# Kernel tuning notes

Measured on AMD Instinct MI355X. Metric: run time of the kernel, lower is better.

Reference implementation:

```python
import jax, jax.numpy as jnp
import numpy as np

N = 50000   # num_nodes
F = 128     # node_features
E = 800000  # num_edges (avg degree 16)


def setup_inputs() -> dict:
    key = jax.random.key(0)
    ks = jax.random.split(key, 12)
    s = 1.0 / np.sqrt(F)
    return {
        "x": jax.random.normal(ks[0], (N, F), jnp.float32),
        "edge_index": jax.random.randint(ks[1], (2, E), 0, N),
        "edge_weight": jax.random.uniform(ks[2], (E,), jnp.float32),
        # TopKPooling projection vector p (PyG stores it as [1, F])
        "p": jax.random.normal(ks[3], (F,), jnp.float32) * s,
        # GRU params, torch gate order (r, z, n)
        "w_ih": jax.random.normal(ks[4], (3 * F, F), jnp.float32) * s,
        "w_hh": jax.random.normal(ks[5], (3 * F, F), jnp.float32) * s,
        "b_ih": jax.random.normal(ks[6], (3 * F,), jnp.float32) * s,
        "b_hh": jax.random.normal(ks[7], (3 * F,), jnp.float32) * s,
        # initial evolving GCN weight [F, F] (glorot-initialized in original)
        "W0": jax.random.normal(ks[8], (F, F), jnp.float32) * s,
        # trailing Linear(F, F)
        "W_lin": jax.random.normal(ks[9], (F, F), jnp.float32) * s,
        "b_lin": jax.random.normal(ks[10], (F,), jnp.float32) * s,
    }


def reference(x, edge_index, edge_weight, p, w_ih, w_hh, b_ih, b_hh, W0, W_lin, b_lin):
    n_nodes, f = x.shape
    # --- TopKPooling: score nodes, select top-F (ratio = F/N) ---
    score = jnp.tanh((x @ p) / jnp.linalg.norm(p))          # [N]
    top_scores, perm = jax.lax.top_k(score, f)              # sorted desc, k = F
    x_tilde = x[perm] * top_scores[:, None]                 # [F, F]
    # --- GRU single step (seq_len=1, batch=F): evolve weight matrix ---
    gi = x_tilde @ w_ih.T + b_ih                            # [F, 3F]
    gh = W0 @ w_hh.T + b_hh                                 # [F, 3F]
    r = jax.nn.sigmoid(gi[:, :f] + gh[:, :f])
    z = jax.nn.sigmoid(gi[:, f:2 * f] + gh[:, f:2 * f])
    n = jnp.tanh(gi[:, 2 * f:] + r * gh[:, 2 * f:])
    W = (1.0 - z) * n + z * W0                              # evolved [F, F]
    # --- GCNConv_Fixed_W: gcn_norm (self-loops, sym norm) + aggregate ---
    loop = jnp.arange(n_nodes)
    row = jnp.concatenate([edge_index[0], loop])            # sources
    col = jnp.concatenate([edge_index[1], loop])            # targets
    ew = jnp.concatenate([edge_weight, jnp.ones((n_nodes,), x.dtype)])
    deg = jax.ops.segment_sum(ew, col, num_segments=n_nodes)
    dinv = jnp.where(deg > 0, jnp.where(deg > 0, deg, 1.0) ** -0.5, 0.0)
    norm = dinv[row] * ew * dinv[col]                       # [E+N]
    xw = x @ W                                              # [N, F]
    h = jax.ops.segment_sum(norm[:, None] * xw[row], col, num_segments=n_nodes)
    # --- relu + Linear ---
    return jax.nn.relu(h) @ W_lin.T + b_lin
```

## Files before the change

kernel.cpp:

```cpp
#include <hip/hip_runtime.h>
#include <hip/hip_fp16.h>

#define NF 128
#define TK 128

typedef _Float16 f16;
typedef f16 half8 __attribute__((ext_vector_type(8)));
typedef float floatx4 __attribute__((ext_vector_type(4)));

__device__ __forceinline__ unsigned okey(float f) {
  unsigned u = __float_as_uint(f);
  return (u & 0x80000000u) ? ~u : (u | 0x80000000u);
}

__device__ __forceinline__ void edge_slice(const int* __restrict__ ei, const float* __restrict__ ew,
                                           unsigned long long* __restrict__ cnt64,
                                           unsigned short* __restrict__ eslot, int E, int e, int elim) {
  if (e < elim) {
    int c = ei[E + e];
    unsigned fx = __float2uint_rn(ew[e] * 16777216.0f);
    unsigned long long old =
        atomicAdd(&cnt64[c], ((unsigned long long)1 << 32) | (unsigned long long)fx);
    eslot[e] = (unsigned short)(old >> 32);
  }
}

__global__ void score_kernel(const float* __restrict__ x, const float* __restrict__ p,
                             float* __restrict__ score, unsigned* __restrict__ keys,
                             unsigned* __restrict__ bins, int n) {
  int t = threadIdx.x;
  int rib = t >> 3;
  int l8 = t & 7;
  int r = blockIdx.x * 32 + rib;
  if (r >= n) return;
  const float4* xr = (const float4*)&x[(size_t)r * NF + l8 * 16];
  const float4* pr = (const float4*)&p[l8 * 16];
  float d = 0.f, pp = 0.f;
#pragma unroll
  for (int i = 0; i < 4; ++i) {
    float4 xv = xr[i];
    float4 pv = pr[i];
    d = fmaf(xv.x, pv.x, d); d = fmaf(xv.y, pv.y, d);
    d = fmaf(xv.z, pv.z, d); d = fmaf(xv.w, pv.w, d);
    pp = fmaf(pv.x, pv.x, pp); pp = fmaf(pv.y, pv.y, pp);
    pp = fmaf(pv.z, pv.z, pp); pp = fmaf(pv.w, pv.w, pp);
  }
#pragma unroll
  for (int off = 4; off > 0; off >>= 1) {
    d += __shfl_down(d, off, 8);
    pp += __shfl_down(pp, off, 8);
  }
  if (l8 == 0) {
    float s = tanhf(d / sqrtf(pp));
    score[r] = s;
    unsigned k = okey(s);
    keys[r] = k;
    atomicAdd(&bins[k >> 16], 1u);
  }
}

__global__ __launch_bounds__(1024) void findbin_edge_kernel(const unsigned* __restrict__ bins,
                                                            unsigned* __restrict__ thrB,
                                                            const int* __restrict__ ei,
                                                            const float* __restrict__ ew,
                                                            unsigned long long* __restrict__ cnt64,
                                                            unsigned short* __restrict__ eslot,
                                                            int E, int ebase, int elim) {
  if (blockIdx.x > 0) {
    edge_slice(ei, ew, cnt64, eslot, E, ebase + ((int)blockIdx.x - 1) * 1024 + (int)threadIdx.x, elim);
    return;
  }
  __shared__ unsigned csum[1024];
  int t = threadIdx.x;
  unsigned hv[64];
  unsigned s = 0;
  const unsigned* bp = bins + t * 64;
#pragma unroll
  for (int b = 0; b < 64; ++b) { hv[b] = bp[b]; s += hv[b]; }
  csum[t] = s;
  __syncthreads();
  for (int st = 1; st < 1024; st <<= 1) {
    unsigned add = (t + st < 1024) ? csum[t + st] : 0u;
    __syncthreads();
    csum[t] += add;
    __syncthreads();
  }
  unsigned mySum = csum[t];
  unsigned above = (t == 1023) ? 0u : csum[t + 1];
  if (mySum >= (unsigned)TK && above < (unsigned)TK) {
    unsigned cum = above;
    int b = 63;
    for (; b > 0; --b) {
      unsigned h = hv[b];
      if (cum + h >= (unsigned)TK) break;
      cum += h;
    }
    thrB[0] = (unsigned)(t * 64 + b);
  }
}

__global__ __launch_bounds__(1024) void compact_edge_kernel(const unsigned* __restrict__ keys,
                                                            const unsigned* __restrict__ thrB,
                                                            int* __restrict__ ncnt,
                                                            int* __restrict__ candIdx, int n, int nOwn,
                                                            const int* __restrict__ ei,
                                                            const float* __restrict__ ew,
                                                            unsigned long long* __restrict__ cnt64,
                                                            unsigned short* __restrict__ eslot,
                                                            int E, int ebase, int elim) {
  if ((int)blockIdx.x >= nOwn) {
    edge_slice(ei, ew, cnt64, eslot, E,
               ebase + ((int)blockIdx.x - nOwn) * 1024 + (int)threadIdx.x, elim);
    return;
  }
  int i = blockIdx.x * 1024 + threadIdx.x;
  if (i < n) {
    if ((keys[i] >> 16) >= thrB[0]) {
      int pos = atomicAdd(ncnt, 1);
      candIdx[pos] = i;
    }
  }
}

#define CCAP 6144
__global__ __launch_bounds__(1024) void select_edge_kernel(const unsigned* __restrict__ keys,
                                                           const int* __restrict__ candIdx,
                                                           const int* __restrict__ ncp,
                                                           const float* __restrict__ score,
                                                           int* __restrict__ perm,
                                                           float* __restrict__ tsc,
                                                           const int* __restrict__ ei,
                                                           const float* __restrict__ ew,
                                                           unsigned long long* __restrict__ cnt64,
                                                           unsigned short* __restrict__ eslot,
                                                           int E, int ebase, int elim) {
  if (blockIdx.x > 0) {
    edge_slice(ei, ew, cnt64, eslot, E, ebase + ((int)blockIdx.x - 1) * 1024 + (int)threadIdx.x, elim);
    return;
  }
  __shared__ unsigned sk[CCAP];
  __shared__ int si[CCAP];
  int nc = ncp[0];
  int t = threadIdx.x;
  int m = nc < CCAP ? nc : CCAP;
  for (int i = t; i < m; i += 1024) {
    int ci = candIdx[i];
    si[i] = ci;
    sk[i] = keys[ci];
  }
  __syncthreads();
  for (int ci = t; ci < nc; ci += 1024) {
    unsigned mk;
    int mi;
    if (ci < CCAP) { mk = sk[ci]; mi = si[ci]; }
    else { mi = candIdx[ci]; mk = keys[mi]; }
    int rank = 0;
    for (int j = 0; j < m; ++j) {
      unsigned kj = sk[j];
      int ij = si[j];
      rank += (kj > mk || (kj == mk && ij < mi)) ? 1 : 0;
    }
    for (int j = CCAP; j < nc; ++j) {
      int ij = candIdx[j];
      unsigned kj = keys[ij];
      rank += (kj > mk || (kj == mk && ij < mi)) ? 1 : 0;
    }
    if (rank < TK) {
      perm[rank] = mi;
      tsc[rank] = score[mi];
    }
  }
}

__global__ void gru_edge_kernel(const float* __restrict__ x, const int* __restrict__ perm,
                                const float* __restrict__ tsc, const float* __restrict__ W0,
                                const float* __restrict__ w_ih, const float* __restrict__ w_hh,
                                const float* __restrict__ b_ih, const float* __restrict__ b_hh,
                                float* __restrict__ WT,
                                const int* __restrict__ ei, const float* __restrict__ ew,
                                unsigned long long* __restrict__ cnt64,
                                unsigned short* __restrict__ eslot, int E, int ebase, int elim) {
  if ((int)blockIdx.x >= NF) {
    edge_slice(ei, ew, cnt64, eslot, E, ebase + ((int)blockIdx.x - NF) * 128 + (int)threadIdx.x, elim);
    return;
  }
  __shared__ float xs[NF], w0s[NF];
  int i = blockIdx.x, j = threadIdx.x;
  int pi = perm[i];
  float s = tsc[i];
  xs[j] = x[(size_t)pi * NF + j] * s;
  w0s[j] = W0[i * NF + j];
  __syncthreads();
  float gir = b_ih[j], giz = b_ih[NF + j], gin = b_ih[2 * NF + j];
  float ghr = b_hh[j], ghz = b_hh[NF + j], ghn = b_hh[2 * NF + j];
  const float* wr = w_ih + (size_t)j * NF;
  const float* wz = w_ih + (size_t)(NF + j) * NF;
  const float* wn = w_ih + (size_t)(2 * NF + j) * NF;
  const float* ur = w_hh + (size_t)j * NF;
  const float* uz = w_hh + (size_t)(NF + j) * NF;
  const float* un = w_hh + (size_t)(2 * NF + j) * NF;
#pragma unroll 4
  for (int k = 0; k < NF; ++k) {
    float xv = xs[k], wv = w0s[k];
    gir = fmaf(xv, wr[k], gir);
    giz = fmaf(xv, wz[k], giz);
    gin = fmaf(xv, wn[k], gin);
    ghr = fmaf(wv, ur[k], ghr);
    ghz = fmaf(wv, uz[k], ghz);
    ghn = fmaf(wv, un[k], ghn);
  }
  float r = 1.0f / (1.0f + expf(-(gir + ghr)));
  float z = 1.0f / (1.0f + expf(-(giz + ghz)));
  float nn = tanhf(gin + r * ghn);
  WT[(size_t)j * NF + i] = (1.0f - z) * nn + z * w0s[j];
}

#define SCAN_B 1024
__global__ __launch_bounds__(1024) void scan1_kernel(const unsigned long long* __restrict__ cnt64,
                                                     int* __restrict__ offL, int* __restrict__ bsum,
                                                     float* __restrict__ dinv, int n) {
  __shared__ int sd[SCAN_B];
  int t = threadIdx.x;
  int i = blockIdx.x * SCAN_B + t;
  int v = 0;
  if (i < n) {
    unsigned long long cv = cnt64[i];
    v = (int)(cv >> 32);
    float dsum = (float)((unsigned)cv) * (1.0f / 16777216.0f) + 1.0f;
    dinv[i] = 1.0f / sqrtf(dsum);
  }
  sd[t] = v;
  __syncthreads();
  for (int s = 1; s < SCAN_B; s <<= 1) {
    int add = (t >= s) ? sd[t - s] : 0;
    __syncthreads();
    sd[t] += add;
    __syncthreads();
  }
  if (i <= n) offL[i] = sd[t] - v;
  if (t == SCAN_B - 1) bsum[blockIdx.x] = sd[t];
}

__global__ void scan2_kernel(const int* __restrict__ bsum, int* __restrict__ bexc, int nb) {
  int t = threadIdx.x;
  if (t < 64) {
    int v = (t < nb) ? bsum[t] : 0;
    int incl = v;
#pragma unroll
    for (int s = 1; s < 64; s <<= 1) {
      int u = __shfl_up(incl, s, 64);
      if (t >= s) incl += u;
    }
    if (t <= nb) bexc[t] = incl - v;
  }
}

__global__ void fill_kernel(const int* __restrict__ ei, const float* __restrict__ ew,
                            const float* __restrict__ dinv, const int* __restrict__ offL,
                            const int* __restrict__ bexc, const unsigned short* __restrict__ eslot,
                            unsigned* __restrict__ epair, int E) {
  int e = blockIdx.x * 256 + threadIdx.x;
  if (e >= E) return;
  int r = ei[e], c = ei[E + e];
  int pos = offL[c] + bexc[c >> 10] + (int)eslot[e];
  float cf = dinv[r] * ew[e] * dinv[c];
  unsigned hb = (unsigned)__builtin_bit_cast(unsigned short, __float2half(cf));
  epair[pos] = (unsigned)r | (hb << 16);
}

__global__ void aggregate_kernel(const unsigned* __restrict__ epair, const int* __restrict__ offL,
                                 const int* __restrict__ bexc, const float* __restrict__ dinv,
                                 const uint4* __restrict__ xw4, unsigned* __restrict__ hh, int n) {
  int w = (int)((blockIdx.x * (size_t)blockDim.x + threadIdx.x) >> 6);
  if (w >= n) return;
  int lane = threadIdx.x & 63;
  int q = lane >> 4, l16 = lane & 15;
  int n0 = offL[w] + bexc[w >> 10];
  int n1 = offL[w + 1] + bexc[(w + 1) >> 10];
  float acc[8] = {0.f, 0.f, 0.f, 0.f, 0.f, 0.f, 0.f, 0.f};
  if (q == 0) {
    float dv = dinv[w];
    float c2 = dv * dv;
    uint4 su = xw4[(size_t)w * 16 + l16];
    float2 f0 = __half22float2(*(const __half2*)&su.x);
    float2 f1 = __half22float2(*(const __half2*)&su.y);
    float2 f2 = __half22float2(*(const __half2*)&su.z);
    float2 f3 = __half22float2(*(const __half2*)&su.w);
    acc[0] = c2 * f0.x; acc[1] = c2 * f0.y; acc[2] = c2 * f1.x; acc[3] = c2 * f1.y;
    acc[4] = c2 * f2.x; acc[5] = c2 * f2.y; acc[6] = c2 * f3.x; acc[7] = c2 * f3.y;
  }
  int e = n0 + q;
  for (; e + 4 < n1; e += 8) {
    unsigned p0 = epair[e], p1 = epair[e + 4];
    uint4 u0 = xw4[(size_t)(p0 & 0xFFFFu) * 16 + l16];
    uint4 u1 = xw4[(size_t)(p1 & 0xFFFFu) * 16 + l16];
    float c0 = __half2float(__builtin_bit_cast(__half, (unsigned short)(p0 >> 16)));
    float c1 = __half2float(__builtin_bit_cast(__half, (unsigned short)(p1 >> 16)));
    float2 f0, f1, f2, f3;
    f0 = __half22float2(*(const __half2*)&u0.x); f1 = __half22float2(*(const __half2*)&u0.y);
    f2 = __half22float2(*(const __half2*)&u0.z); f3 = __half22float2(*(const __half2*)&u0.w);
    acc[0] = fmaf(c0, f0.x, acc[0]); acc[1] = fmaf(c0, f0.y, acc[1]);
    acc[2] = fmaf(c0, f1.x, acc[2]); acc[3] = fmaf(c0, f1.y, acc[3]);
    acc[4] = fmaf(c0, f2.x, acc[4]); acc[5] = fmaf(c0, f2.y, acc[5]);
    acc[6] = fmaf(c0, f3.x, acc[6]); acc[7] = fmaf(c0, f3.y, acc[7]);
    f0 = __half22float2(*(const __half2*)&u1.x); f1 = __half22float2(*(const __half2*)&u1.y);
    f2 = __half22float2(*(const __half2*)&u1.z); f3 = __half22float2(*(const __half2*)&u1.w);
    acc[0] = fmaf(c1, f0.x, acc[0]); acc[1] = fmaf(c1, f0.y, acc[1]);
    acc[2] = fmaf(c1, f1.x, acc[2]); acc[3] = fmaf(c1, f1.y, acc[3]);
    acc[4] = fmaf(c1, f2.x, acc[4]); acc[5] = fmaf(c1, f2.y, acc[5]);
    acc[6] = fmaf(c1, f3.x, acc[6]); acc[7] = fmaf(c1, f3.y, acc[7]);
  }
  for (; e < n1; e += 4) {
    unsigned p0 = epair[e];
    uint4 u0 = xw4[(size_t)(p0 & 0xFFFFu) * 16 + l16];
    float c0 = __half2float(__builtin_bit_cast(__half, (unsigned short)(p0 >> 16)));
    float2 f0 = __half22float2(*(const __half2*)&u0.x);
    float2 f1 = __half22float2(*(const __half2*)&u0.y);
    float2 f2 = __half22float2(*(const __half2*)&u0.z);
    float2 f3 = __half22float2(*(const __half2*)&u0.w);
    acc[0] = fmaf(c0, f0.x, acc[0]); acc[1] = fmaf(c0, f0.y, acc[1]);
    acc[2] = fmaf(c0, f1.x, acc[2]); acc[3] = fmaf(c0, f1.y, acc[3]);
    acc[4] = fmaf(c0, f2.x, acc[4]); acc[5] = fmaf(c0, f2.y, acc[5]);
    acc[6] = fmaf(c0, f3.x, acc[6]); acc[7] = fmaf(c0, f3.y, acc[7]);
  }
#pragma unroll
  for (int j = 0; j < 8; ++j) {
    float a = acc[j];
    a += __shfl_xor(a, 16, 64);
    a += __shfl_xor(a, 32, 64);
    acc[j] = a;
  }
  if (q == 0) {
    __half2 h0 = __floats2half2_rn(fmaxf(acc[0], 0.f), fmaxf(acc[1], 0.f));
    __half2 h1 = __floats2half2_rn(fmaxf(acc[2], 0.f), fmaxf(acc[3], 0.f));
    __half2 h2 = __floats2half2_rn(fmaxf(acc[4], 0.f), fmaxf(acc[5], 0.f));
    __half2 h3 = __floats2half2_rn(fmaxf(acc[6], 0.f), fmaxf(acc[7], 0.f));
    uint4 o;
    o.x = *(unsigned*)&h0; o.y = *(unsigned*)&h1; o.z = *(unsigned*)&h2; o.w = *(unsigned*)&h3;
    *(uint4*)&hh[(size_t)w * 64 + l16 * 4] = o;
  }
}

template <int HIN, int HOUT, int BIAS>
__global__ __launch_bounds__(256) void gemm_mfma_kernel(const void* __restrict__ Ap,
                                                        const float* __restrict__ Bt,
                                                        const float* __restrict__ bias,
                                                        void* __restrict__ Cp, int nrows) {
  __shared__ char ldsA[64 * 256];
  __shared__ char ldsB[128 * 256];
  const int t = threadIdx.x;
  const int row0 = blockIdx.x * 64;
  {
    const float2* B2 = (const float2*)Bt;
#pragma unroll
    for (int i = 0; i < 32; ++i) {
      int idx = i * 256 + t;
      int nn = idx >> 6, kp = idx & 63;
      float2 v = B2[idx];
      __half2 h = __floats2half2_rn(v.x, v.y);
      int byte = (nn * 256 + kp * 4) ^ ((nn & 7) << 4);
      *(unsigned*)&ldsB[byte] = *(unsigned*)&h;
    }
  }
  if (HIN) {
    const unsigned* Ah = (const unsigned*)Ap;
#pragma unroll
    for (int i = 0; i < 16; ++i) {
      int idx = i * 256 + t;
      int r = idx >> 6, cp = idx & 63;
      int gr = row0 + r;
      unsigned v = (gr < nrows) ? Ah[(size_t)gr * 64 + cp] : 0u;
      int byte = (r * 256 + cp * 4) ^ ((r & 7) << 4);
      *(unsigned*)&ldsA[byte] = v;
    }
  } else {
    const float2* A2 = (const float2*)Ap;
#pragma unroll
    for (int i = 0; i < 16; ++i) {
      int idx = i * 256 + t;
      int r = idx >> 6, cp = idx & 63;
      int gr = row0 + r;
      float2 v = make_float2(0.f, 0.f);
      if (gr < nrows) v = A2[(size_t)gr * 64 + cp];
      __half2 h = __floats2half2_rn(v.x, v.y);
      int byte = (r * 256 + cp * 4) ^ ((r & 7) << 4);
      *(unsigned*)&ldsA[byte] = *(unsigned*)&h;
    }
  }
  __syncthreads();
  const int wave = t >> 6, l = t & 63;
  const int wr0 = wave * 16;
  const int lm = l & 15, q = l >> 4;
  floatx4 acc[8];
#pragma unroll
  for (int nt = 0; nt < 8; ++nt) acc[nt] = (floatx4){0.f, 0.f, 0.f, 0.f};
#pragma unroll
  for (int ks = 0; ks < 4; ++ks) {
    int arow = wr0 + lm;
    half8 a = *(const half8*)&ldsA[(arow * 256 + ks * 64 + q * 16) ^ ((arow & 7) << 4)];
#pragma unroll
    for (int nt = 0; nt < 8; ++nt) {
      int nn = nt * 16 + lm;
      half8 b = *(const half8*)&ldsB[(nn * 256 + ks * 64 + q * 16) ^ ((nn & 7) << 4)];
      acc[nt] = __builtin_amdgcn_mfma_f32_16x16x32_f16(a, b, acc[nt], 0, 0, 0);
    }
  }
#pragma unroll
  for (int nt = 0; nt < 8; ++nt) {
    int col = nt * 16 + lm;
    float bv = BIAS ? bias[col] : 0.f;
#pragma unroll
    for (int r = 0; r < 4; ++r) {
      int gr = row0 + wr0 + q * 4 + r;
      if (gr < nrows) {
        float v = acc[nt][r] + bv;
        if (HOUT) ((__half*)Cp)[(size_t)gr * NF + col] = __float2half(v);
        else ((float*)Cp)[(size_t)gr * NF + col] = v;
      }
    }
  }
}

extern "C" void kernel_launch(void* const* d_in, const int* in_sizes, int n_in,
                              void* d_out, int out_size, void* d_ws, size_t ws_size,
                              hipStream_t stream) {
  const float* x = (const float*)d_in[0];
  const int* ei = (const int*)d_in[1];
  const float* ew = (const float*)d_in[2];
  const float* p = (const float*)d_in[3];
  const float* w_ih = (const float*)d_in[4];
  const float* w_hh = (const float*)d_in[5];
  const float* b_ih = (const float*)d_in[6];
  const float* b_hh = (const float*)d_in[7];
  const float* W0 = (const float*)d_in[8];
  const float* W_lin = (const float*)d_in[9];
  const float* b_lin = (const float*)d_in[10];
  float* out = (float*)d_out;

  const int N = in_sizes[0] / NF;
  const int E = in_sizes[1] / 2;

  char* w = (char*)d_ws;
  unsigned* xwh = (unsigned*)w;
  unsigned* hh = xwh + (size_t)N * 64;
  float* score = (float*)(hh + (size_t)N * 64);
  unsigned* keys = (unsigned*)(score + N);
  unsigned long long* cnt64 = (unsigned long long*)(keys + N);
  unsigned* bins = (unsigned*)(cnt64 + N);
  int* ncnt = (int*)(bins + 65536);
  float* dinv = (float*)(ncnt + 1);
  unsigned* thrB = (unsigned*)(dinv + N);
  int* candIdx = (int*)(thrB + 1);
  int* offL = candIdx + N;
  int* bsum = offL + N + 1;
  int* bexc = bsum + 64;
  unsigned short* eslot = (unsigned short*)(bexc + 64);
  unsigned* epair = (unsigned*)(eslot + E);
  float* WevT = (float*)(epair + E);
  int* perm = (int*)(WevT + NF * NF);
  float* tsc = (float*)(perm + NF);

  const int nb = (N + SCAN_B - 1) / SCAN_B;
  const int nbEdge = (E + 255) / 256;
  const int nbGemm = (N + 63) / 64;
  const int nOwnC = (N + 1023) / 1024;

  const int per = (E + 3) / 4;
  const int bA = (per + 1023) / 1024;
  const int eA0 = 0, eA1 = (bA * 1024 < E) ? bA * 1024 : E;
  const int bB = (per + 1023) / 1024;
  const int eB0 = eA1, eB1 = (eB0 + bB * 1024 < E) ? eB0 + bB * 1024 : E;
  const int bC = (per + 1023) / 1024;
  const int eC0 = eB1, eC1 = (eC0 + bC * 1024 < E) ? eC0 + bC * 1024 : E;
  const int eD0 = eC1;
  const int bD = (E - eD0 + 127) / 128;

  hipMemsetAsync(cnt64, 0, (size_t)N * 8 + 65536 * 4 + 4, stream);
  score_kernel<<<(N + 31) / 32, 256, 0, stream>>>(x, p, score, keys, bins, N);
  findbin_edge_kernel<<<1 + bA, 1024, 0, stream>>>(bins, thrB, ei, ew, cnt64, eslot, E, eA0, eA1);
  compact_edge_kernel<<<nOwnC + bB, 1024, 0, stream>>>(keys, thrB, ncnt, candIdx, N, nOwnC,
                                                       ei, ew, cnt64, eslot, E, eB0, eB1);
  select_edge_kernel<<<1 + bC, 1024, 0, stream>>>(keys, candIdx, ncnt, score, perm, tsc,
                                                  ei, ew, cnt64, eslot, E, eC0, eC1);
  gru_edge_kernel<<<NF + bD, NF, 0, stream>>>(x, perm, tsc, W0, w_ih, w_hh, b_ih, b_hh, WevT,
                                              ei, ew, cnt64, eslot, E, eD0, E);
  gemm_mfma_kernel<0, 1, 0><<<nbGemm, 256, 0, stream>>>(x, WevT, nullptr, xwh, N);
  scan1_kernel<<<nb, SCAN_B, 0, stream>>>(cnt64, offL, bsum, dinv, N);
  scan2_kernel<<<1, 64, 0, stream>>>(bsum, bexc, nb);
  fill_kernel<<<nbEdge, 256, 0, stream>>>(ei, ew, dinv, offL, bexc, eslot, epair, E);
  aggregate_kernel<<<(N + 3) / 4, 256, 0, stream>>>(epair, offL, bexc, dinv,
                                                    (const uint4*)xwh, hh, N);
  gemm_mfma_kernel<1, 0, 1><<<nbGemm, 256, 0, stream>>>(hh, W_lin, b_lin, out, N);
}
```

Before: 212.6 us.

## Fuse edge work into score and GEMM kernels and replace memset with kernel

The edge degree-counting slices are rebalanced so that most edges (three fifths) ride along with the score kernel, and the rest are split across the top-k stages. The first GEMM (x @ W) is merged with the CSR fill pass into one launch with separate block ranges, so the two independent workloads run concurrently. hipMemsetAsync is replaced by a grid-stride zero kernel. The aim is fewer launches and filling the idle or serial phases with edge work. In exchange, blocks within a launch become heterogeneous and LDS use is reserved even by fill blocks.

```diff
diff --git a/kernel.cpp b/kernel.cpp
--- a/kernel.cpp
+++ b/kernel.cpp
@@ -25,9 +25,24 @@
   }
 }
 
-__global__ void score_kernel(const float* __restrict__ x, const float* __restrict__ p,
-                             float* __restrict__ score, unsigned* __restrict__ keys,
-                             unsigned* __restrict__ bins, int n) {
+__global__ void zero_kernel(uint4* __restrict__ dst, int n4) {
+  int i = blockIdx.x * blockDim.x + threadIdx.x;
+  int stride = gridDim.x * blockDim.x;
+  uint4 z = make_uint4(0u, 0u, 0u, 0u);
+  for (; i < n4; i += stride) dst[i] = z;
+}
+
+__global__ void score_edge_kernel(const float* __restrict__ x, const float* __restrict__ p,
+                                  float* __restrict__ score, unsigned* __restrict__ keys,
+                                  unsigned* __restrict__ bins, int n, int nbScore,
+                                  const int* __restrict__ ei, const float* __restrict__ ew,
+                                  unsigned long long* __restrict__ cnt64,
+                                  unsigned short* __restrict__ eslot, int E, int ebase, int elim) {
+  if ((int)blockIdx.x >= nbScore) {
+    edge_slice(ei, ew, cnt64, eslot, E,
+               ebase + ((int)blockIdx.x - nbScore) * 256 + (int)threadIdx.x, elim);
+    return;
+  }
   int t = threadIdx.x;
   int rib = t >> 3;
   int l8 = t & 7;
@@ -255,17 +270,86 @@
   }
 }
 
-__global__ void fill_kernel(const int* __restrict__ ei, const float* __restrict__ ew,
-                            const float* __restrict__ dinv, const int* __restrict__ offL,
-                            const int* __restrict__ bexc, const unsigned short* __restrict__ eslot,
-                            unsigned* __restrict__ epair, int E) {
-  int e = blockIdx.x * 256 + threadIdx.x;
-  if (e >= E) return;
-  int r = ei[e], c = ei[E + e];
-  int pos = offL[c] + bexc[c >> 10] + (int)eslot[e];
-  float cf = dinv[r] * ew[e] * dinv[c];
-  unsigned hb = (unsigned)__builtin_bit_cast(unsigned short, __float2half(cf));
-  epair[pos] = (unsigned)r | (hb << 16);
+__global__ __launch_bounds__(256) void gemm1_fill_kernel(const float* __restrict__ x,
+                                                         const float* __restrict__ Bt,
+                                                         unsigned* __restrict__ Ch, int nrows,
+                                                         int nbGemm,
+                                                         const int* __restrict__ ei,
+                                                         const float* __restrict__ ew,
+                                                         const float* __restrict__ dinv,
+                                                         const int* __restrict__ offL,
+                                                         const int* __restrict__ bexc,
+                                                         const unsigned short* __restrict__ eslot,
+                                                         unsigned* __restrict__ epair, int E) {
+  __shared__ char ldsA[64 * 256];
+  __shared__ char ldsB[128 * 256];
+  if ((int)blockIdx.x >= nbGemm) {
+    int e = ((int)blockIdx.x - nbGemm) * 256 + (int)threadIdx.x;
+    if (e < E) {
+      int r = ei[e], c = ei[E + e];
+      int pos = offL[c] + bexc[c >> 10] + (int)eslot[e];
+      float cf = dinv[r] * ew[e] * dinv[c];
+      unsigned hb = (unsigned)__builtin_bit_cast(unsigned short, __float2half(cf));
+      epair[pos] = (unsigned)r | (hb << 16);
+    }
+    return;
+  }
+  const int t = threadIdx.x;
+  const int row0 = blockIdx.x * 64;
+  {
+    const float2* B2 = (const float2*)Bt;
+#pragma unroll
+    for (int i = 0; i < 32; ++i) {
+      int idx = i * 256 + t;
+      int nn = idx >> 6, kp = idx & 63;
+      float2 v = B2[idx];
+      __half2 h = __floats2half2_rn(v.x, v.y);
+      int byte = (nn * 256 + kp * 4) ^ ((nn & 7) << 4);
+      *(unsigned*)&ldsB[byte] = *(unsigned*)&h;
+    }
+  }
+  {
+    const float2* A2 = (const float2*)x;
+#pragma unroll
+    for (int i = 0; i < 16; ++i) {
+      int idx = i * 256 + t;
+      int r = idx >> 6, cp = idx & 63;
+      int gr = row0 + r;
+      float2 v = make_float2(0.f, 0.f);
+      if (gr < nrows) v = A2[(size_t)gr * 64 + cp];
+      __half2 h = __floats2half2_rn(v.x, v.y);
+      int byte = (r * 256 + cp * 4) ^ ((r & 7) << 4);
+      *(unsigned*)&ldsA[byte] = *(unsigned*)&h;
+    }
+  }
+  __syncthreads();
+  const int wave = t >> 6, l = t & 63;
+  const int wr0 = wave * 16;
+  const int lm = l & 15, q = l >> 4;
+  floatx4 acc[8];
+#pragma unroll
+  for (int nt = 0; nt < 8; ++nt) acc[nt] = (floatx4){0.f, 0.f, 0.f, 0.f};
+#pragma unroll
+  for (int ks = 0; ks < 4; ++ks) {
+    int arow = wr0 + lm;
+    half8 a = *(const half8*)&ldsA[(arow * 256 + ks * 64 + q * 16) ^ ((arow & 7) << 4)];
+#pragma unroll
+    for (int nt = 0; nt < 8; ++nt) {
+      int nn = nt * 16 + lm;
+      half8 b = *(const half8*)&ldsB[(nn * 256 + ks * 64 + q * 16) ^ ((nn & 7) << 4)];
+      acc[nt] = __builtin_amdgcn_mfma_f32_16x16x32_f16(a, b, acc[nt], 0, 0, 0);
+    }
+  }
+#pragma unroll
+  for (int nt = 0; nt < 8; ++nt) {
+    int col = nt * 16 + lm;
+#pragma unroll
+    for (int r = 0; r < 4; ++r) {
+      int gr = row0 + wr0 + q * 4 + r;
+      if (gr < nrows)
+        ((__half*)Ch)[(size_t)gr * NF + col] = __float2half(acc[nt][r]);
+    }
+  }
 }
 
 __global__ void aggregate_kernel(const unsigned* __restrict__ epair, const int* __restrict__ offL,
@@ -463,31 +547,36 @@
   const int nb = (N + SCAN_B - 1) / SCAN_B;
   const int nbEdge = (E + 255) / 256;
   const int nbGemm = (N + 63) / 64;
+  const int nbScore = (N + 31) / 32;
   const int nOwnC = (N + 1023) / 1024;
 
-  const int per = (E + 3) / 4;
-  const int bA = (per + 1023) / 1024;
-  const int eA0 = 0, eA1 = (bA * 1024 < E) ? bA * 1024 : E;
-  const int bB = (per + 1023) / 1024;
-  const int eB0 = eA1, eB1 = (eB0 + bB * 1024 < E) ? eB0 + bB * 1024 : E;
-  const int bC = (per + 1023) / 1024;
-  const int eC0 = eB1, eC1 = (eC0 + bC * 1024 < E) ? eC0 + bC * 1024 : E;
-  const int eD0 = eC1;
-  const int bD = (E - eD0 + 127) / 128;
-
-  hipMemsetAsync(cnt64, 0, (size_t)N * 8 + 65536 * 4 + 4, stream);
-  score_kernel<<<(N + 31) / 32, 256, 0, stream>>>(x, p, score, keys, bins, N);
-  findbin_edge_kernel<<<1 + bA, 1024, 0, stream>>>(bins, thrB, ei, ew, cnt64, eslot, E, eA0, eA1);
-  compact_edge_kernel<<<nOwnC + bB, 1024, 0, stream>>>(keys, thrB, ncnt, candIdx, N, nOwnC,
-                                                       ei, ew, cnt64, eslot, E, eB0, eB1);
-  select_edge_kernel<<<1 + bC, 1024, 0, stream>>>(keys, candIdx, ncnt, score, perm, tsc,
-                                                  ei, ew, cnt64, eslot, E, eC0, eC1);
-  gru_edge_kernel<<<NF + bD, NF, 0, stream>>>(x, perm, tsc, W0, w_ih, w_hh, b_ih, b_hh, WevT,
-                                              ei, ew, cnt64, eslot, E, eD0, E);
-  gemm_mfma_kernel<0, 1, 0><<<nbGemm, 256, 0, stream>>>(x, WevT, nullptr, xwh, N);
+  const int eA1 = (int)(((long long)E * 3) / 5);
+  const int perR = (E - eA1 + 3) / 4;
+  const int eB1 = (eA1 + perR < E) ? eA1 + perR : E;
+  const int eC1 = (eB1 + perR < E) ? eB1 + perR : E;
+  const int eD1 = (eC1 + perR < E) ? eC1 + perR : E;
+  const int bSA = (eA1 + 255) / 256;
+  const int bSB = (eB1 - eA1 + 1023) / 1024;
+  const int bSC = (eC1 - eB1 + 1023) / 1024;
+  const int bSD = (eD1 - eC1 + 1023) / 1024;
+  const int bSE = (E - eD1 + 127) / 128;
+
+  const int n4zero = (N * 8 + 65536 * 4 + 4 + 15) / 16;
+
+  zero_kernel<<<64, 1024, 0, stream>>>((uint4*)cnt64, n4zero);
+  score_edge_kernel<<<nbScore + bSA, 256, 0, stream>>>(x, p, score, keys, bins, N, nbScore,
+                                                       ei, ew, cnt64, eslot, E, 0, eA1);
+  findbin_edge_kernel<<<1 + bSB, 1024, 0, stream>>>(bins, thrB, ei, ew, cnt64, eslot, E, eA1, eB1);
+  compact_edge_kernel<<<nOwnC + bSC, 1024, 0, stream>>>(keys, thrB, ncnt, candIdx, N, nOwnC,
+                                                        ei, ew, cnt64, eslot, E, eB1, eC1);
+  select_edge_kernel<<<1 + bSD, 1024, 0, stream>>>(keys, candIdx, ncnt, score, perm, tsc,
+                                                   ei, ew, cnt64, eslot, E, eC1, eD1);
+  gru_edge_kernel<<<NF + bSE, NF, 0, stream>>>(x, perm, tsc, W0, w_ih, w_hh, b_ih, b_hh, WevT,
+                                               ei, ew, cnt64, eslot, E, eD1, E);
   scan1_kernel<<<nb, SCAN_B, 0, stream>>>(cnt64, offL, bsum, dinv, N);
   scan2_kernel<<<1, 64, 0, stream>>>(bsum, bexc, nb);
-  fill_kernel<<<nbEdge, 256, 0, stream>>>(ei, ew, dinv, offL, bexc, eslot, epair, E);
+  gemm1_fill_kernel<<<nbGemm + nbEdge, 256, 0, stream>>>(x, WevT, xwh, N, nbGemm,
+                                                         ei, ew, dinv, offL, bexc, eslot, epair, E);
   aggregate_kernel<<<(N + 3) / 4, 256, 0, stream>>>(epair, offL, bexc, dinv,
                                                     (const uint4*)xwh, hh, N);
   gemm_mfma_kernel<1, 0, 1><<<nbGemm, 256, 0, stream>>>(hh, W_lin, b_lin, out, N);
```

Result: faster. 198.7 us (-6.5%).
